# Kernel tuning notes

Measured on AMD Instinct MI355X. Metric: run time of the kernel, lower is better.

Reference implementation:

```python
import jax, jax.numpy as jnp
import numpy as np

B, S, H = 2, 2048, 1024
NH, HD = 16, 64
SCALE = HD ** -0.5


def setup_inputs() -> dict:
    key = jax.random.key(0)
    k1, k2, k3, k4 = jax.random.split(key, 4)
    hidden_states = jax.random.normal(k1, (B, S, H), dtype=jnp.float32)
    attention_mask = jax.random.randint(k2, (B, S), 0, 2, dtype=jnp.int32)
    # xavier-uniform-ish init scale
    w_qkv = jax.random.normal(k3, (3 * H, H), dtype=jnp.float32) * (2.0 / (H + 3 * H)) ** 0.5
    w_out = jax.random.normal(k4, (H, H), dtype=jnp.float32) * (1.0 / H) ** 0.5
    return {"hidden_states": hidden_states, "attention_mask": attention_mask,
            "w_qkv": w_qkv, "w_out": w_out}


def reference(hidden_states, attention_mask, w_qkv, w_out):
    b, s, _ = hidden_states.shape
    qkv = hidden_states @ w_qkv.T                      # [B,S,3H]
    q, k, v = jnp.split(qkv, 3, axis=-1)
    # [B,S,H] -> [B,NH,S,HD]
    reshape = lambda x: x.reshape(b, s, NH, HD).transpose(0, 2, 1, 3)
    q, k, v = reshape(q), reshape(k), reshape(v)
    scores = jnp.einsum('bhqd,bhkd->bhqk', q, k) * SCALE   # [B,NH,S,S]
    mask = attention_mask[:, None, None, :] == 0           # [B,1,1,S]
    scores = jnp.where(mask, -jnp.inf, scores)
    attn = jax.nn.softmax(scores, axis=-1)                 # dropout p: eval mode -> identity
    out = jnp.einsum('bhqk,bhkd->bhqd', attn, v)           # [B,NH,S,HD]
    out = out.transpose(0, 2, 1, 3).reshape(b, s, H)
    return out @ w_out.T
```

## Files before the change

kernel.cpp:

```cpp
#include <hip/hip_runtime.h>
#include <string.h>


typedef __bf16    bf16x8 __attribute__((ext_vector_type(8)));
typedef _Float16  f16x4  __attribute__((ext_vector_type(4)));
typedef _Float16  f16x2  __attribute__((ext_vector_type(2)));
typedef float     f32x4  __attribute__((ext_vector_type(4)));

#define NTOK   4096
#define HDIM   1024
#define SEQ    2048
#define NHEAD  16
#define F2SHIFT 4.0f
#define QSCALE  0.18033688f
#define LSTRIDE 68
#define KHALF  1024

__device__ __forceinline__ float bf2f(unsigned short u) {
    union { unsigned int i; float f; } x;
    x.i = ((unsigned int)u) << 16;
    return x.f;
}
__device__ __forceinline__ unsigned short f2bf(float f) {
    union { __bf16 h; unsigned short u; } x;
    x.h = (__bf16)f;
    return x.u;
}
__device__ __forceinline__ unsigned short f2h(float f) {
    union { _Float16 h; unsigned short u; } x;
    x.h = (_Float16)f;
    return x.u;
}
__device__ __forceinline__ float h2f(unsigned short u) {
    union { unsigned short u; _Float16 h; } x;
    x.u = u;
    return (float)x.h;
}
__device__ __forceinline__ f16x2 pkrtz(float a, float b) {
    union { __fp16 __attribute__((ext_vector_type(2))) i; f16x2 o; } x;
    x.i = __builtin_amdgcn_cvt_pkrtz(a, b);
    return x.o;
}

__device__ __forceinline__ int detect_f32(const unsigned short* hs) {
    unsigned int idx = (threadIdx.x & 63) * 4096u;
    float f = bf2f(hs[idx]);
    return __any(!(fabsf(f) < 1e4f));
}

typedef const __attribute__((address_space(1))) unsigned int* gptr_u32;
typedef __attribute__((address_space(3))) unsigned int* lptr_u32;

__device__ __forceinline__ void async16(const unsigned short* g, unsigned short* l) {
    __builtin_amdgcn_global_load_lds((gptr_u32)g, (lptr_u32)l, 16, 0, 0);
}

__global__ void convert3_kernel(const void* __restrict__ s0, const void* __restrict__ s1,
                                const void* __restrict__ s2, unsigned short* __restrict__ dst) {
    const int isf32 = detect_f32((const unsigned short*)s0);
    if (!isf32) return;
    int g = blockIdx.x * blockDim.x + threadIdx.x;
    const int stride = gridDim.x * blockDim.x;
    for (; g < 1048576; g += stride) {
        int i = g * 8;
        const void* src; int off;
        if (i < 4194304)      { src = s0; off = i; }
        else if (i < 7340032) { src = s1; off = i - 4194304; }
        else                  { src = s2; off = i - 7340032; }
        const float* s = (const float*)src + off;
        unsigned short o[8];
#pragma unroll
        for (int j = 0; j < 8; j++) o[j] = f2bf(s[j]);
        *(uint4*)(dst + i) = *(const uint4*)o;
    }
}

__global__ __launch_bounds__(256) void gemm_qkv(
    const unsigned short* __restrict__ Xc, const unsigned short* __restrict__ Wc,
    const unsigned short* __restrict__ Xraw, const unsigned short* __restrict__ Wraw,
    unsigned short* __restrict__ q_out, unsigned short* __restrict__ k_out,
    unsigned short* __restrict__ v_out) {
    const int K = 1024;
    __shared__ __align__(16) unsigned short Xs0[128 * 32];
    __shared__ __align__(16) unsigned short Xs1[128 * 32];
    __shared__ __align__(16) unsigned short Ws0[128 * 32];
    __shared__ __align__(16) unsigned short Ws1[128 * 32];

    const int isf32 = detect_f32(Xraw);
    const unsigned short* X = isf32 ? Xc : Xraw;
    const unsigned short* W = isf32 ? Wc : Wraw;

    const int t = threadIdx.x;
    const int w = t >> 6, lane = t & 63, quad = lane >> 4, lr = lane & 15;
    const int wrow = (w >> 1) * 64, wcol = (w & 1) * 64;

    const int hid = blockIdx.x;
    const int xcd = hid & 7, r = hid >> 3;
    const int by = xcd * 4 + r / 24;
    const int bx = r % 24;
    const int m0 = by * 128, n0 = bx * 128;
    const bool vblk = (n0 >= 2048);

    f32x4 acc[4][4];
#pragma unroll
    for (int mi = 0; mi < 4; mi++)
#pragma unroll
        for (int ni = 0; ni < 4; ni++) acc[mi][ni] = (f32x4){0.f, 0.f, 0.f, 0.f};

    const int srow = w * 32 + (lane >> 2);
    const int scol = (lane & 3) * 8;
    const unsigned short* xg = X + (size_t)(m0 + srow) * K + scol;
    const unsigned short* wg = W + (size_t)(n0 + srow) * K + scol;
    unsigned short* xl0 = &Xs0[w * 1024];
    unsigned short* xl1 = &Xs1[w * 1024];
    unsigned short* wl0 = &Ws0[w * 1024];
    unsigned short* wl1 = &Ws1[w * 1024];

    async16(xg, xl0);
    async16(xg + 16 * K, xl0 + 512);
    async16(wg, wl0);
    async16(wg + 16 * K, wl0 + 512);

#define QKV_COMPUTE(Xh, Wh)                                                            \
    {                                                                                  \
        bf16x8 af[4], bfr[4];                                                          \
        _Pragma("unroll")                                                              \
        for (int mi = 0; mi < 4; mi++)                                                 \
            af[mi] = *(const bf16x8*)&Xh[(wrow + mi * 16 + lr) * 32 + quad * 8];       \
        _Pragma("unroll")                                                              \
        for (int ni = 0; ni < 4; ni++)                                                 \
            bfr[ni] = *(const bf16x8*)&Wh[(wcol + ni * 16 + lr) * 32 + quad * 8];      \
        __builtin_amdgcn_s_setprio(1);                                                 \
        if (!vblk) {                                                                   \
            _Pragma("unroll")                                                          \
            for (int mi = 0; mi < 4; mi++)                                             \
                _Pragma("unroll")                                                      \
                for (int ni = 0; ni < 4; ni++)                                         \
                    acc[mi][ni] = __builtin_amdgcn_mfma_f32_16x16x32_bf16(             \
                        af[mi], bfr[ni], acc[mi][ni], 0, 0, 0);                        \
        } else {                                                                       \
            _Pragma("unroll")                                                          \
            for (int mi = 0; mi < 4; mi++)                                             \
                _Pragma("unroll")                                                      \
                for (int ni = 0; ni < 4; ni++)                                         \
                    acc[mi][ni] = __builtin_amdgcn_mfma_f32_16x16x32_bf16(             \
                        bfr[ni], af[mi], acc[mi][ni], 0, 0, 0);                        \
        }                                                                              \
        __builtin_amdgcn_s_setprio(0);                                                 \
    }

    for (int k0 = 0; k0 < K; k0 += 64) {
        __syncthreads();
        async16(xg + k0 + 32, xl1);
        async16(xg + k0 + 32 + 16 * K, xl1 + 512);
        async16(wg + k0 + 32, wl1);
        async16(wg + k0 + 32 + 16 * K, wl1 + 512);
        QKV_COMPUTE(Xs0, Ws0);

        __syncthreads();
        if (k0 + 64 < K) {
            async16(xg + k0 + 64, xl0);
            async16(xg + k0 + 64 + 16 * K, xl0 + 512);
            async16(wg + k0 + 64, wl0);
            async16(wg + k0 + 64 + 16 * K, wl0 + 512);
        }
        QKV_COMPUTE(Xs1, Ws1);
    }
#undef QKV_COMPUTE

    if (!vblk) {
#pragma unroll
        for (int mi = 0; mi < 4; mi++)
#pragma unroll
            for (int ni = 0; ni < 4; ni++)
#pragma unroll
                for (int rr = 0; rr < 4; rr++) {
                    int mrow = m0 + wrow + mi * 16 + quad * 4 + rr;
                    int j = n0 + wcol + ni * 16 + lr;
                    float val = acc[mi][ni][rr];
                    int which = j >> 10, rem = j & 1023;
                    int nh = rem >> 6, hd = rem & 63;
                    int b = mrow >> 11, s = mrow & 2047;
                    size_t dst = ((size_t)(b * NHEAD + nh) * SEQ + s) * 64 + hd;
                    if (which == 0) q_out[dst] = f2bf(val * QSCALE);
                    else            k_out[dst] = f2bf(val);
                }
    } else {
#pragma unroll
        for (int mi = 0; mi < 4; mi++)
#pragma unroll
            for (int ni = 0; ni < 4; ni++)
#pragma unroll
                for (int rr = 0; rr < 4; rr++) {
                    int n = n0 + wcol + ni * 16 + quad * 4 + rr;
                    int m = m0 + wrow + mi * 16 + lr;
                    float val = acc[mi][ni][rr];
                    int rem = n & 1023;
                    int nh = rem >> 6, hd = rem & 63;
                    int b = m >> 11, s = m & 2047;
                    size_t dst = ((size_t)(b * NHEAD + nh) * 64 + hd) * SEQ + s;
                    v_out[dst] = f2h(val);
                }
    }
}

__global__ __launch_bounds__(256) void gemm_out(
    const unsigned short* __restrict__ X, const unsigned short* __restrict__ Wc,
    const unsigned short* __restrict__ Wraw,
    void* __restrict__ d_out, const unsigned short* __restrict__ hs_raw) {
    const int K = 1024, N = 1024;
    __shared__ __align__(16) unsigned short Xs0[64 * 32];
    __shared__ __align__(16) unsigned short Xs1[64 * 32];
    __shared__ __align__(16) unsigned short Xs2[64 * 32];
    __shared__ __align__(16) unsigned short Xs3[64 * 32];
    __shared__ __align__(16) unsigned short Ws0[128 * 32];
    __shared__ __align__(16) unsigned short Ws1[128 * 32];
    __shared__ __align__(16) unsigned short Ws2[128 * 32];
    __shared__ __align__(16) unsigned short Ws3[128 * 32];

    const int isf32 = detect_f32(hs_raw);
    const unsigned short* W = isf32 ? Wc : Wraw;

    const int t = threadIdx.x;
    const int w = t >> 6, lane = t & 63, quad = lane >> 4, lr = lane & 15;
    const int wrow = (w >> 1) * 32, wcol = (w & 1) * 64;
    const int m0 = blockIdx.y * 64, n0 = blockIdx.x * 128;

    f32x4 acc[2][4];
#pragma unroll
    for (int mi = 0; mi < 2; mi++)
#pragma unroll
        for (int ni = 0; ni < 4; ni++) acc[mi][ni] = (f32x4){0.f, 0.f, 0.f, 0.f};

    const int sxrow = w * 16 + (lane >> 2);
    const int swrow = w * 32 + (lane >> 2);
    const int scol = (lane & 3) * 8;
    const unsigned short* xg = X + (size_t)(m0 + sxrow) * K + scol;
    const unsigned short* wg = W + (size_t)(n0 + swrow) * K + scol;
    unsigned short* xl[4] = { &Xs0[w * 512], &Xs1[w * 512], &Xs2[w * 512], &Xs3[w * 512] };
    unsigned short* wl[4] = { &Ws0[w * 1024], &Ws1[w * 1024], &Ws2[w * 1024], &Ws3[w * 1024] };

    for (int k0 = 0; k0 < K; k0 += 128) {
        __syncthreads();
#pragma unroll
        for (int j = 0; j < 4; j++) {
            async16(xg + k0 + j * 32, xl[j]);
            async16(wg + k0 + j * 32, wl[j]);
            async16(wg + k0 + j * 32 + 16 * K, wl[j] + 512);
        }
        __syncthreads();
#pragma unroll
        for (int h = 0; h < 4; h++) {
            const unsigned short* Xh = (h == 0) ? Xs0 : (h == 1) ? Xs1 : (h == 2) ? Xs2 : Xs3;
            const unsigned short* Wh = (h == 0) ? Ws0 : (h == 1) ? Ws1 : (h == 2) ? Ws2 : Ws3;
            bf16x8 af[2], bfr[4];
#pragma unroll
            for (int mi = 0; mi < 2; mi++)
                af[mi] = *(const bf16x8*)&Xh[(wrow + mi * 16 + lr) * 32 + quad * 8];
#pragma unroll
            for (int ni = 0; ni < 4; ni++)
                bfr[ni] = *(const bf16x8*)&Wh[(wcol + ni * 16 + lr) * 32 + quad * 8];
#pragma unroll
            for (int mi = 0; mi < 2; mi++)
#pragma unroll
                for (int ni = 0; ni < 4; ni++)
                    acc[mi][ni] = __builtin_amdgcn_mfma_f32_16x16x32_bf16(af[mi], bfr[ni], acc[mi][ni], 0, 0, 0);
        }
    }

#pragma unroll
    for (int mi = 0; mi < 2; mi++)
#pragma unroll
        for (int ni = 0; ni < 4; ni++)
#pragma unroll
            for (int rr = 0; rr < 4; rr++) {
                int mrow = m0 + wrow + mi * 16 + quad * 4 + rr;
                int j = n0 + wcol + ni * 16 + lr;
                float val = acc[mi][ni][rr];
                size_t dst = (size_t)mrow * N + j;
                if (isf32) ((float*)d_out)[dst] = val;
                else ((unsigned short*)d_out)[dst] = f2bf(val);
            }
}

__global__ __launch_bounds__(256, 2) void flash_attn_v13(
    const unsigned short* __restrict__ q, const unsigned short* __restrict__ k,
    const unsigned short* __restrict__ vt, const int* __restrict__ mask,
    unsigned short* __restrict__ attn_out,
    unsigned short* __restrict__ opart, float* __restrict__ lpart,
    const int kbase) {
    __shared__ __align__(16) unsigned short Ks[128 * LSTRIDE];
    __shared__ __align__(16) unsigned short Vt0[64 * LSTRIDE];
    __shared__ __align__(16) unsigned short Vt1[64 * LSTRIDE];
    __shared__ __align__(16) float Msk[136];

    const int t = threadIdx.x;
    const int w = t >> 6, lane = t & 63, quad = lane >> 4, lr = lane & 15;
    const int bh = blockIdx.x, b = bh >> 4, h = bh & 15;
    const int q0 = blockIdx.y * 128;

    const unsigned short* qb = q + (size_t)bh * SEQ * 64;
    const unsigned short* kb = k + (size_t)bh * SEQ * 64;
    const unsigned short* vtb = vt + (size_t)bh * 64 * SEQ;
    const int* mb = mask + b * SEQ;

    bf16x8 qf[2][2];
#pragma unroll
    for (int qg = 0; qg < 2; qg++) {
        const unsigned short* qrow = qb + (size_t)(q0 + w * 32 + qg * 16 + lr) * 64 + quad * 8;
        qf[qg][0] = *(const bf16x8*)qrow;
        qf[qg][1] = *(const bf16x8*)(qrow + 32);
    }

    f32x4 oacc[2][4];
#pragma unroll
    for (int qg = 0; qg < 2; qg++)
#pragma unroll
        for (int dt = 0; dt < 4; dt++) oacc[qg][dt] = (f32x4){0.f, 0.f, 0.f, 0.f};
    float l_st[2] = {0.f, 0.f};

    const int sr = t >> 2;
    const int sc = (t & 3) * 16;

    for (int kk0 = kbase; kk0 < kbase + KHALF; kk0 += 128) {
        const uint4* kp0 = (const uint4*)(kb + (size_t)(kk0 + sr) * 64 + sc);
        const uint4* kp1 = (const uint4*)(kb + (size_t)(kk0 + 64 + sr) * 64 + sc);
        const uint4* vp0 = (const uint4*)(vtb + (size_t)sr * SEQ + kk0 + sc);
        const uint4* vp1 = (const uint4*)(vtb + (size_t)sr * SEQ + kk0 + 64 + sc);
        uint4 k0a = kp0[0], k0b = kp0[1];
        uint4 k1a = kp1[0], k1b = kp1[1];
        uint4 v0a = vp0[0], v0b = vp0[1];
        uint4 v1a = vp1[0], v1b = vp1[1];
        float mval = 0.f;
        if (t < 128) mval = (mb[kk0 + t] == 0) ? -1e30f : -F2SHIFT;

        __syncthreads();
        *(uint4*)&Ks[sr * LSTRIDE + sc] = k0a;
        *(uint4*)&Ks[sr * LSTRIDE + sc + 8] = k0b;
        *(uint4*)&Ks[(64 + sr) * LSTRIDE + sc] = k1a;
        *(uint4*)&Ks[(64 + sr) * LSTRIDE + sc + 8] = k1b;
        *(uint4*)&Vt0[sr * LSTRIDE + sc] = v0a;
        *(uint4*)&Vt0[sr * LSTRIDE + sc + 8] = v0b;
        *(uint4*)&Vt1[sr * LSTRIDE + sc] = v1a;
        *(uint4*)&Vt1[sr * LSTRIDE + sc + 8] = v1b;
        if (t < 128) Msk[t] = mval;
        __syncthreads();

        __builtin_amdgcn_s_setprio(1);
#pragma unroll
        for (int mt = 0; mt < 8; mt++) {
            bf16x8 a1h0 = *(bf16x8*)&Ks[(mt * 16 + lr) * LSTRIDE + quad * 8];
            bf16x8 a1h1 = *(bf16x8*)&Ks[(mt * 16 + lr) * LSTRIDE + 32 + quad * 8];
            const unsigned short* vb_ = (mt < 4) ? Vt0 : Vt1;
            const int mcol = (mt & 3) * 16;
            f16x4 a2[4];
#pragma unroll
            for (int dt = 0; dt < 4; dt++)
                a2[dt] = *(const f16x4*)&vb_[(dt * 16 + lr) * LSTRIDE + mcol + quad * 4];
            float4 mv = *(const float4*)&Msk[mt * 16 + quad * 4];
            f32x4 zi = (f32x4){mv.x, mv.y, mv.z, mv.w};

#pragma unroll
            for (int qg = 0; qg < 2; qg++) {
                f32x4 z = __builtin_amdgcn_mfma_f32_16x16x32_bf16(a1h0, qf[qg][0], zi, 0, 0, 0);
                z = __builtin_amdgcn_mfma_f32_16x16x32_bf16(a1h1, qf[qg][1], z, 0, 0, 0);
                float p0 = __builtin_amdgcn_exp2f(z[0]);
                float p1 = __builtin_amdgcn_exp2f(z[1]);
                float p2 = __builtin_amdgcn_exp2f(z[2]);
                float p3 = __builtin_amdgcn_exp2f(z[3]);
                l_st[qg] += (p0 + p1) + (p2 + p3);
                f16x2 ab = pkrtz(p0, p1);
                f16x2 cd = pkrtz(p2, p3);
                f16x4 b2;
                b2[0] = ab[0]; b2[1] = ab[1]; b2[2] = cd[0]; b2[3] = cd[1];
#pragma unroll
                for (int dt = 0; dt < 4; dt++)
                    oacc[qg][dt] = __builtin_amdgcn_mfma_f32_16x16x16f16(a2[dt], b2, oacc[qg][dt], 0, 0, 0);
            }
        }
        __builtin_amdgcn_s_setprio(0);
    }

    float lsum[2];
#pragma unroll
    for (int qg = 0; qg < 2; qg++) {
        float s = l_st[qg];
        s += __shfl_xor(s, 16);
        s += __shfl_xor(s, 32);
        lsum[qg] = s;
    }

    if (kbase == 0) {
#pragma unroll
        for (int qg = 0; qg < 2; qg++) {
            const int qrow = q0 + w * 32 + qg * 16 + lr;
            if (quad == 0) lpart[bh * 2048 + qrow] = lsum[qg];
            size_t tok = (size_t)(b * SEQ + qrow);
#pragma unroll
            for (int dt = 0; dt < 4; dt++)
#pragma unroll
                for (int rr = 0; rr < 4; rr++)
                    opart[tok * HDIM + h * 64 + dt * 16 + quad * 4 + rr] =
                        f2h(oacc[qg][dt][rr]);
        }
    } else {
#pragma unroll
        for (int qg = 0; qg < 2; qg++) {
            const int qrow = q0 + w * 32 + qg * 16 + lr;
            const float inv = 1.0f / (lsum[qg] + lpart[bh * 2048 + qrow]);
            size_t tok = (size_t)(b * SEQ + qrow);
#pragma unroll
            for (int dt = 0; dt < 4; dt++) {
                const unsigned short* op = &opart[tok * HDIM + h * 64 + dt * 16 + quad * 4];
#pragma unroll
                for (int rr = 0; rr < 4; rr++)
                    attn_out[tok * HDIM + h * 64 + dt * 16 + quad * 4 + rr] =
                        f2bf((oacc[qg][dt][rr] + h2f(op[rr])) * inv);
            }
        }
    }
}

extern "C" void kernel_launch(void* const* d_in, const int* in_sizes, int n_in,
                              void* d_out, int out_size, void* d_ws, size_t ws_size,
                              hipStream_t stream) {
    const void* hs_raw = d_in[0];
    const int* mask = (const int*)d_in[1];
    const void* wqkv_raw = d_in[2];
    const void* wout_raw = d_in[3];

    char* wsb = (char*)d_ws;
    unsigned short* hs_c = (unsigned short*)(wsb + 256);
    unsigned short* wqkv_c = hs_c + 4194304;
    unsigned short* wout_c = wqkv_c + 3145728;
    unsigned short* qw = wout_c + 1048576;
    unsigned short* kw = qw + 4194304;
    unsigned short* vtw = kw + 4194304;
    unsigned short* ao = vtw + 4194304;

    unsigned short* opart = hs_c;
    float* lpart = (float*)wqkv_c;

    convert3_kernel<<<1024, 256, 0, stream>>>(hs_raw, wqkv_raw, wout_raw, hs_c);

    gemm_qkv<<<768, 256, 0, stream>>>(hs_c, wqkv_c,
                                      (const unsigned short*)hs_raw,
                                      (const unsigned short*)wqkv_raw,
                                      qw, kw, vtw);
    flash_attn_v13<<<dim3(32, 16), 256, 0, stream>>>(qw, kw, vtw, mask, ao, opart, lpart, 0);
    flash_attn_v13<<<dim3(32, 16), 256, 0, stream>>>(qw, kw, vtw, mask, ao, opart, lpart, 1024);
    gemm_out<<<dim3(8, 64), 256, 0, stream>>>(ao, wout_c,
                                              (const unsigned short*)wout_raw, d_out,
                                              (const unsigned short*)hs_raw);
}
```

Baseline: 192.0 us.

## Merge split-K attention into one pass and double-buffer output GEMM loads

```diff
diff --git a/kernel.cpp b/kernel.cpp
--- a/kernel.cpp
+++ b/kernel.cpp
@@ -14,7 +14,6 @@
 #define F2SHIFT 4.0f
 #define QSCALE  0.18033688f
 #define LSTRIDE 68
-#define KHALF  1024
 
 __device__ __forceinline__ float bf2f(unsigned short u) {
     union { unsigned int i; float f; } x;
@@ -30,11 +29,6 @@
     union { _Float16 h; unsigned short u; } x;
     x.h = (_Float16)f;
     return x.u;
-}
-__device__ __forceinline__ float h2f(unsigned short u) {
-    union { unsigned short u; _Float16 h; } x;
-    x.u = u;
-    return (float)x.h;
 }
 __device__ __forceinline__ f16x2 pkrtz(float a, float b) {
     union { __fp16 __attribute__((ext_vector_type(2))) i; f16x2 o; } x;
@@ -211,12 +205,8 @@
     const int K = 1024, N = 1024;
     __shared__ __align__(16) unsigned short Xs0[64 * 32];
     __shared__ __align__(16) unsigned short Xs1[64 * 32];
-    __shared__ __align__(16) unsigned short Xs2[64 * 32];
-    __shared__ __align__(16) unsigned short Xs3[64 * 32];
     __shared__ __align__(16) unsigned short Ws0[128 * 32];
     __shared__ __align__(16) unsigned short Ws1[128 * 32];
-    __shared__ __align__(16) unsigned short Ws2[128 * 32];
-    __shared__ __align__(16) unsigned short Ws3[128 * 32];
 
     const int isf32 = detect_f32(hs_raw);
     const unsigned short* W = isf32 ? Wc : Wraw;
@@ -237,36 +227,50 @@
     const int scol = (lane & 3) * 8;
     const unsigned short* xg = X + (size_t)(m0 + sxrow) * K + scol;
     const unsigned short* wg = W + (size_t)(n0 + swrow) * K + scol;
-    unsigned short* xl[4] = { &Xs0[w * 512], &Xs1[w * 512], &Xs2[w * 512], &Xs3[w * 512] };
-    unsigned short* wl[4] = { &Ws0[w * 1024], &Ws1[w * 1024], &Ws2[w * 1024], &Ws3[w * 1024] };
-
-    for (int k0 = 0; k0 < K; k0 += 128) {
-        __syncthreads();
-#pragma unroll
-        for (int j = 0; j < 4; j++) {
-            async16(xg + k0 + j * 32, xl[j]);
-            async16(wg + k0 + j * 32, wl[j]);
-            async16(wg + k0 + j * 32 + 16 * K, wl[j] + 512);
+    unsigned short* xl0 = &Xs0[w * 512];
+    unsigned short* xl1 = &Xs1[w * 512];
+    unsigned short* wl0 = &Ws0[w * 1024];
+    unsigned short* wl1 = &Ws1[w * 1024];
+
+    async16(xg, xl0);
+    async16(wg, wl0);
+    async16(wg + 16 * K, wl0 + 512);
+
+#define OUT_COMPUTE(Xh, Wh)                                                            \
+    {                                                                                  \
+        bf16x8 af[2], bfr[4];                                                          \
+        _Pragma("unroll")                                                              \
+        for (int mi = 0; mi < 2; mi++)                                                 \
+            af[mi] = *(const bf16x8*)&Xh[(wrow + mi * 16 + lr) * 32 + quad * 8];       \
+        _Pragma("unroll")                                                              \
+        for (int ni = 0; ni < 4; ni++)                                                 \
+            bfr[ni] = *(const bf16x8*)&Wh[(wcol + ni * 16 + lr) * 32 + quad * 8];      \
+        __builtin_amdgcn_s_setprio(1);                                                 \
+        _Pragma("unroll")                                                              \
+        for (int mi = 0; mi < 2; mi++)                                                 \
+            _Pragma("unroll")                                                          \
+            for (int ni = 0; ni < 4; ni++)                                             \
+                acc[mi][ni] = __builtin_amdgcn_mfma_f32_16x16x32_bf16(                 \
+                    af[mi], bfr[ni], acc[mi][ni], 0, 0, 0);                            \
+        __builtin_amdgcn_s_setprio(0);                                                 \
+    }
+
+    for (int k0 = 0; k0 < K; k0 += 64) {
+        __syncthreads();
+        async16(xg + k0 + 32, xl1);
+        async16(wg + k0 + 32, wl1);
+        async16(wg + k0 + 32 + 16 * K, wl1 + 512);
+        OUT_COMPUTE(Xs0, Ws0);
+
+        __syncthreads();
+        if (k0 + 64 < K) {
+            async16(xg + k0 + 64, xl0);
+            async16(wg + k0 + 64, wl0);
+            async16(wg + k0 + 64 + 16 * K, wl0 + 512);
         }
-        __syncthreads();
-#pragma unroll
-        for (int h = 0; h < 4; h++) {
-            const unsigned short* Xh = (h == 0) ? Xs0 : (h == 1) ? Xs1 : (h == 2) ? Xs2 : Xs3;
-            const unsigned short* Wh = (h == 0) ? Ws0 : (h == 1) ? Ws1 : (h == 2) ? Ws2 : Ws3;
-            bf16x8 af[2], bfr[4];
-#pragma unroll
-            for (int mi = 0; mi < 2; mi++)
-                af[mi] = *(const bf16x8*)&Xh[(wrow + mi * 16 + lr) * 32 + quad * 8];
-#pragma unroll
-            for (int ni = 0; ni < 4; ni++)
-                bfr[ni] = *(const bf16x8*)&Wh[(wcol + ni * 16 + lr) * 32 + quad * 8];
-#pragma unroll
-            for (int mi = 0; mi < 2; mi++)
-#pragma unroll
-                for (int ni = 0; ni < 4; ni++)
-                    acc[mi][ni] = __builtin_amdgcn_mfma_f32_16x16x32_bf16(af[mi], bfr[ni], acc[mi][ni], 0, 0, 0);
-        }
-    }
+        OUT_COMPUTE(Xs1, Ws1);
+    }
+#undef OUT_COMPUTE
 
 #pragma unroll
     for (int mi = 0; mi < 2; mi++)
@@ -283,12 +287,10 @@
             }
 }
 
-__global__ __launch_bounds__(256, 2) void flash_attn_v13(
+__global__ __launch_bounds__(256, 2) void flash_attn_v12(
     const unsigned short* __restrict__ q, const unsigned short* __restrict__ k,
     const unsigned short* __restrict__ vt, const int* __restrict__ mask,
-    unsigned short* __restrict__ attn_out,
-    unsigned short* __restrict__ opart, float* __restrict__ lpart,
-    const int kbase) {
+    unsigned short* __restrict__ attn_out) {
     __shared__ __align__(16) unsigned short Ks[128 * LSTRIDE];
     __shared__ __align__(16) unsigned short Vt0[64 * LSTRIDE];
     __shared__ __align__(16) unsigned short Vt1[64 * LSTRIDE];
@@ -322,7 +324,7 @@
     const int sr = t >> 2;
     const int sc = (t & 3) * 16;
 
-    for (int kk0 = kbase; kk0 < kbase + KHALF; kk0 += 128) {
+    for (int kk0 = 0; kk0 < SEQ; kk0 += 128) {
         const uint4* kp0 = (const uint4*)(kb + (size_t)(kk0 + sr) * 64 + sc);
         const uint4* kp1 = (const uint4*)(kb + (size_t)(kk0 + 64 + sr) * 64 + sc);
         const uint4* vp0 = (const uint4*)(vtb + (size_t)sr * SEQ + kk0 + sc);
@@ -381,43 +383,23 @@
         __builtin_amdgcn_s_setprio(0);
     }
 
-    float lsum[2];
+    float inv[2];
 #pragma unroll
     for (int qg = 0; qg < 2; qg++) {
         float s = l_st[qg];
         s += __shfl_xor(s, 16);
         s += __shfl_xor(s, 32);
-        lsum[qg] = s;
-    }
-
-    if (kbase == 0) {
-#pragma unroll
-        for (int qg = 0; qg < 2; qg++) {
-            const int qrow = q0 + w * 32 + qg * 16 + lr;
-            if (quad == 0) lpart[bh * 2048 + qrow] = lsum[qg];
-            size_t tok = (size_t)(b * SEQ + qrow);
-#pragma unroll
-            for (int dt = 0; dt < 4; dt++)
-#pragma unroll
-                for (int rr = 0; rr < 4; rr++)
-                    opart[tok * HDIM + h * 64 + dt * 16 + quad * 4 + rr] =
-                        f2h(oacc[qg][dt][rr]);
-        }
-    } else {
-#pragma unroll
-        for (int qg = 0; qg < 2; qg++) {
-            const int qrow = q0 + w * 32 + qg * 16 + lr;
-            const float inv = 1.0f / (lsum[qg] + lpart[bh * 2048 + qrow]);
-            size_t tok = (size_t)(b * SEQ + qrow);
-#pragma unroll
-            for (int dt = 0; dt < 4; dt++) {
-                const unsigned short* op = &opart[tok * HDIM + h * 64 + dt * 16 + quad * 4];
-#pragma unroll
-                for (int rr = 0; rr < 4; rr++)
-                    attn_out[tok * HDIM + h * 64 + dt * 16 + quad * 4 + rr] =
-                        f2bf((oacc[qg][dt][rr] + h2f(op[rr])) * inv);
-            }
-        }
+        inv[qg] = 1.0f / s;
+    }
+#pragma unroll
+    for (int qg = 0; qg < 2; qg++) {
+        size_t tok = (size_t)(b * SEQ + q0 + w * 32 + qg * 16 + lr);
+#pragma unroll
+        for (int dt = 0; dt < 4; dt++)
+#pragma unroll
+            for (int rr = 0; rr < 4; rr++)
+                attn_out[tok * HDIM + h * 64 + dt * 16 + quad * 4 + rr] =
+                    f2bf(oacc[qg][dt][rr] * inv[qg]);
     }
 }
 
@@ -438,17 +420,13 @@
     unsigned short* vtw = kw + 4194304;
     unsigned short* ao = vtw + 4194304;
 
-    unsigned short* opart = hs_c;
-    float* lpart = (float*)wqkv_c;
-
     convert3_kernel<<<1024, 256, 0, stream>>>(hs_raw, wqkv_raw, wout_raw, hs_c);
 
     gemm_qkv<<<768, 256, 0, stream>>>(hs_c, wqkv_c,
                                       (const unsigned short*)hs_raw,
                                       (const unsigned short*)wqkv_raw,
                                       qw, kw, vtw);
-    flash_attn_v13<<<dim3(32, 16), 256, 0, stream>>>(qw, kw, vtw, mask, ao, opart, lpart, 0);
-    flash_attn_v13<<<dim3(32, 16), 256, 0, stream>>>(qw, kw, vtw, mask, ao, opart, lpart, 1024);
+    flash_attn_v12<<<dim3(32, 16), 256, 0, stream>>>(qw, kw, vtw, mask, ao);
     gemm_out<<<dim3(8, 64), 256, 0, stream>>>(ao, wout_c,
                                               (const unsigned short*)wout_raw, d_out,
                                               (const unsigned short*)hs_raw);
```

Measured after the change: 183.2 us. 4.6% less time.
